# Performance work log

Measured on AMD Instinct MI355X. Metric: run time of the kernel, lower is better.

The kernel has to match this reference:

```python
import jax, jax.numpy as jnp
import numpy as np

EPS = 1e-7
BLOCK_SIZE = 128
LN_EPS = 1e-6

def _project(x):
    norm = jnp.maximum(jnp.linalg.norm(x, axis=-1, keepdims=True), EPS)
    max_norm = 1.0 - EPS
    return jnp.where(norm >= 1.0, x / norm * max_norm, x)

def _mobius_add(x, y, c):
    x2 = jnp.sum(x * x, -1, keepdims=True)
    y2 = jnp.sum(y * y, -1, keepdims=True)
    xy = jnp.sum(x * y, -1, keepdims=True)
    num = (1 + 2 * c * xy + c * y2) * x + (1 - c * x2) * y
    den = 1 + 2 * c * xy + c * c * x2 * y2
    return _project(num / jnp.maximum(den, EPS))

def _logmap0(y, c):
    sqrt_c = jnp.maximum(jnp.sqrt(c), EPS)
    y_norm = jnp.linalg.norm(y, axis=-1, keepdims=True)
    safe = jnp.maximum(y_norm, EPS)
    mag = jnp.arctanh(jnp.minimum(y_norm, 1.0 - EPS)) / sqrt_c
    return jnp.where(y_norm < EPS, jnp.zeros_like(y), mag * (y / safe))

def _expmap0(v, c):
    sqrt_c = jnp.maximum(jnp.sqrt(c), EPS)
    v_norm = jnp.linalg.norm(v, axis=-1, keepdims=True)
    safe = jnp.maximum(v_norm, EPS)
    mag = jnp.tanh(sqrt_c * safe) / sqrt_c
    return _project(jnp.where(v_norm < EPS, jnp.zeros_like(v), mag * (v / safe)))

def _dist(x, y, c):
    sqrt_c = jnp.maximum(jnp.sqrt(c), EPS)
    add_norm = jnp.linalg.norm(_mobius_add(-x, y, c), axis=-1)
    sc = jnp.squeeze(sqrt_c, -1)
    arg = jnp.minimum(sc * add_norm, 1.0 - EPS)
    return 2.0 * jnp.arctanh(arg) / sc

def _layernorm(t, scale, bias):
    mu = jnp.mean(t, -1, keepdims=True)
    var = jnp.mean((t - mu) ** 2, -1, keepdims=True)
    return (t - mu) * jax.lax.rsqrt(var + LN_EPS) * scale + bias

def _rope(x, fc):
    # x: [Be, H, bs, hd]; fc: [bs, hd//2] complex
    x_r, x_i = jnp.split(x, 2, -1)
    xc = jax.lax.complex(x_r, x_i)
    rot = xc * fc.reshape(1, 1, fc.shape[0], fc.shape[1])
    return jnp.concatenate([rot.real, rot.imag], -1)

def setup_inputs() -> dict:
    key = jax.random.key(0)
    ks = jax.random.split(key, 8)
    B, N, D, H = 1, 1024, 1024, 16
    w = lambda k, s: jax.random.normal(k, s, jnp.float32) * 0.02
    x = jax.random.normal(ks[0], (B, N, D), jnp.float32) * 0.02  # points inside the ball
    c_global = jax.random.uniform(ks[1], (B, 1), jnp.float32, minval=0.1, maxval=1.0)
    return dict(
        x=x, c_global=c_global,
        qkv_w=w(ks[2], (D, 3 * D)), qkv_b=jnp.zeros((3 * D,), jnp.float32),
        out_w=w(ks[3], (D, D)), out_b=jnp.zeros((D,), jnp.float32),
        ffn_w1=w(ks[4], (D, 4 * D)), ffn_b1=jnp.zeros((4 * D,), jnp.float32),
        ffn_w2=w(ks[5], (4 * D, D)), ffn_b2=jnp.zeros((D,), jnp.float32),
        ln1_scale=jnp.ones((D,), jnp.float32), ln1_bias=jnp.zeros((D,), jnp.float32),
        ln2_scale=jnp.ones((D,), jnp.float32), ln2_bias=jnp.zeros((D,), jnp.float32),
        c_logits=jnp.zeros((H,), jnp.float32),
        geo_scale=jnp.ones((1, H, 1, 1), jnp.float32),
        start_pos=0,
    )

def reference(x, c_global, qkv_w, qkv_b, out_w, out_b, ffn_w1, ffn_b1, ffn_w2, ffn_b2,
              ln1_scale, ln1_bias, ln2_scale, ln2_bias, c_logits, geo_scale, start_pos):
    B, N, D = x.shape
    H = c_logits.shape[0]
    hd = D // H
    bs = BLOCK_SIZE
    nb = N // bs
    Be = B * nb
    xb = x.reshape(Be, bs, D)
    c_b = jnp.repeat(c_global, nb, axis=0).reshape(Be, 1, 1)
    x_res1 = xb
    # tangent-space norm 1 + attention input
    x_norm = _expmap0(_layernorm(_logmap0(xb, c_b), ln1_scale, ln1_bias), c_b)
    x_tan = _logmap0(x_norm, c_b)
    qkv = (x_tan @ qkv_w + qkv_b).reshape(Be, bs, 3, H, hd).transpose(2, 0, 3, 1, 4)
    q, k, v = qkv[0], qkv[1], qkv[2]  # [Be, H, bs, hd]
    # block-local RoPE (module recomputes freqs_cis for h_dim/block_size internally)
    freqs = 1.0 / (10000.0 ** (jnp.arange(0, hd, 2, dtype=jnp.float32) / hd))
    fc = jnp.exp(1j * jnp.outer(jnp.arange(bs), freqs))
    q = _rope(q, fc)
    k = _rope(k, fc)
    c_head = jax.nn.softplus(c_logits).reshape(1, H, 1, 1)
    q_hyp = _expmap0(q, c_head)
    k_hyp = _expmap0(k, c_head)
    d = _dist(q_hyp[:, :, :, None, :], k_hyp[:, :, None, :, :], c_head[:, :, None, :, :])  # [Be,H,bs,bs]
    attn = jax.nn.softmax(-geo_scale * d, axis=-1)
    ao = jnp.einsum('bhqk,bhkd->bhqd', attn, v).transpose(0, 2, 1, 3).reshape(Be, bs, D)
    ao = ao @ out_w + out_b
    x_att = _mobius_add(x_res1, _expmap0(ao, c_b), c_b)
    # tangent-space norm 2 + hyperbolic FFN
    x_norm2 = _expmap0(_layernorm(_logmap0(x_att, c_b), ln2_scale, ln2_bias), c_b)
    t = _logmap0(x_norm2, c_b)
    t = jax.nn.gelu(t @ ffn_w1 + ffn_b1) @ ffn_w2 + ffn_b2
    x_ffn = _expmap0(t, c_b)
    out = _mobius_add(x_att, x_ffn, c_b)
    return out.reshape(B, N, D)
```

## Files before the change

kernel.cpp:

```cpp
#include <hip/hip_runtime.h>

typedef unsigned int uint;
typedef unsigned short ushort;
typedef __attribute__((ext_vector_type(8))) short bf16x8;
typedef __attribute__((ext_vector_type(4))) float f32x4;

#define EPSF 1e-7f
#define ONE_M_EPS 0.99999988079071044921875f
#define ATANH_1ME 8.4056213f
#define Y2_CLIP 0.99999982f

__device__ __forceinline__ ushort f2bf(float f){
  union{float f;uint u;}x; x.f=f; uint u=x.u;
  return (ushort)((u + 0x7fffu + ((u>>16)&1u)) >> 16);
}
__device__ __forceinline__ float bf2f(ushort u){
  union{uint u;float f;}x; x.u = ((uint)u)<<16; return x.f;
}
__device__ __forceinline__ float atanh_c(float a){
  a = fminf(a, ONE_M_EPS);
  return 0.5f*__logf((1.f+a)/(1.f-a));
}
__device__ __forceinline__ float gelu_t(float v){
  return 0.5f*v*(1.f + tanhf(0.7978845608f*(v + 0.044715f*v*v*v)));
}

__device__ __forceinline__ float expmap_factor(float n2, float sc, float& r2){
  float n = sqrtf(n2);
  if (n < EPSF) { r2 = 0.f; return 0.f; }
  float mag = tanhf(sc*n)/sc;
  float f = mag/n;
  if (mag >= 1.f) { f *= ONE_M_EPS/mag; r2 = Y2_CLIP; }
  else r2 = mag*mag;
  return f;
}
__device__ __forceinline__ float roundtrip_factor(float tn2, float sc){
  float tn = sqrtf(tn2);
  if (tn < EPSF) return 0.f;
  float mag = tanhf(sc*tn)/sc;
  if (mag >= 1.f) {
    return ATANH_1ME / (sc * tn);
  } else {
    if (mag < EPSF) return 0.f;
    return (mag/tn) * (atanh_c(mag) / (sc * mag));
  }
}

__device__ __constant__ float FREQS[32] = {
  1.0f, 0.7498942093324559f, 0.5623413251903491f, 0.4216965034285822f,
  0.31622776601683794f, 0.23713737056616552f, 0.1778279410038923f, 0.13335214321633242f,
  0.1f, 0.07498942093324558f, 0.05623413251903491f, 0.04216965034285822f,
  0.03162277660168379f, 0.023713737056616554f, 0.01778279410038923f, 0.013335214321633242f,
  0.01f, 0.007498942093324559f, 0.005623413251903491f, 0.004216965034285822f,
  0.0031622776601683794f, 0.0023713737056616554f, 0.0017782794100389228f, 0.0013335214321633241f,
  0.001f, 0.0007498942093324558f, 0.0005623413251903491f, 0.0004216965034285822f,
  0.00031622776601683794f, 0.00023713737056616553f, 0.00017782794100389227f, 0.00013335214321633243f
};

__device__ __forceinline__ float blkSum(float v, float* tmp){
  #pragma unroll
  for (int o=32;o>0;o>>=1) v += __shfl_xor(v, o, 64);
  int w = threadIdx.x >> 6;
  if ((threadIdx.x & 63) == 0) tmp[w] = v;
  __syncthreads();
  v = tmp[0]+tmp[1]+tmp[2]+tmp[3];
  __syncthreads();
  return v;
}
__device__ __forceinline__ float2 blkSum2(float a, float b, float* tmp){
  #pragma unroll
  for (int o=32;o>0;o>>=1){ a += __shfl_xor(a, o, 64); b += __shfl_xor(b, o, 64); }
  int w = threadIdx.x >> 6;
  if ((threadIdx.x & 63) == 0){ tmp[w] = a; tmp[4+w] = b; }
  __syncthreads();
  float2 r; r.x = tmp[0]+tmp[1]+tmp[2]+tmp[3]; r.y = tmp[4]+tmp[5]+tmp[6]+tmp[7];
  __syncthreads();
  return r;
}

__global__ __launch_bounds__(256) void k_pre(const float* __restrict__ qkv_w,
    const float* __restrict__ out_w, const float* __restrict__ ffn_w1,
    const float* __restrict__ ffn_w2, const float* __restrict__ x,
    const float* __restrict__ cg, const float* __restrict__ lns, const float* __restrict__ lnb,
    ushort* __restrict__ wq, ushort* __restrict__ wo,
    ushort* __restrict__ w1, ushort* __restrict__ w2, ushort* __restrict__ xtan){
  __shared__ float s[32][33];
  int b = blockIdx.x;
  if (b < 12288){
    const float* W; ushort* WT; int K, N;
    if (b < 3072){ W=qkv_w; WT=wq; K=1024; N=3072; }
    else if (b < 4096){ b-=3072; W=out_w; WT=wo; K=1024; N=1024; }
    else if (b < 8192){ b-=4096; W=ffn_w1; WT=w1; K=1024; N=4096; }
    else { b-=8192; W=ffn_w2; WT=w2; K=4096; N=1024; }
    int nbn = N >> 5;
    int n0 = (b % nbn)*32, k0 = (b / nbn)*32;
    int tx = threadIdx.x & 31, ty = threadIdx.x >> 5;
    #pragma unroll
    for (int i=0;i<4;i++)
      s[ty+8*i][tx] = W[(size_t)(k0+ty+8*i)*N + n0+tx];
    __syncthreads();
    #pragma unroll
    for (int i=0;i<4;i++)
      WT[(size_t)(n0+ty+8*i)*K + k0+tx] = f2bf(s[tx][ty+8*i]);
  } else {
    float* tmp = &s[0][0];
    int r = b - 12288, t = threadIdx.x;
    float c = cg[0];
    float sc = fmaxf(sqrtf(c), EPSF);
    float4 xv = ((const float4*)(x + (size_t)r*1024))[t];
    float n2 = blkSum(xv.x*xv.x + xv.y*xv.y + xv.z*xv.z + xv.w*xv.w, tmp);
    float n = sqrtf(n2);
    float f1 = (n < EPSF) ? 0.f : (atanh_c(n) / sc / n);
    float ux = xv.x*f1, uy = xv.y*f1, uz = xv.z*f1, uw = xv.w*f1;
    float2 s12 = blkSum2(ux+uy+uz+uw, ux*ux+uy*uy+uz*uz+uw*uw, tmp);
    float mu = s12.x*(1.f/1024.f);
    float var = s12.y*(1.f/1024.f) - mu*mu;
    float inv = rsqrtf(var + 1e-6f);
    float4 sv = ((const float4*)lns)[t];
    float4 bv = ((const float4*)lnb)[t];
    float ta = (ux-mu)*inv*sv.x + bv.x;
    float tb = (uy-mu)*inv*sv.y + bv.y;
    float tc = (uz-mu)*inv*sv.z + bv.z;
    float td = (uw-mu)*inv*sv.w + bv.w;
    float tn2 = blkSum(ta*ta+tb*tb+tc*tc+td*td, tmp);
    float f = roundtrip_factor(tn2, sc);
    ushort4 o; o.x=f2bf(ta*f); o.y=f2bf(tb*f); o.z=f2bf(tc*f); o.w=f2bf(td*f);
    ((ushort4*)(xtan + (size_t)r*1024))[t] = o;
  }
}

template<int EPI>
__global__ __launch_bounds__(256) void k_gemm(const ushort* __restrict__ A,
    const ushort* __restrict__ Bt, const float* __restrict__ bias,
    void* __restrict__ C, int M, int N, int Kstride, int Kchunk){
  constexpr int MF = 2, NF = 4;
  __shared__ ushort As[2][128*64];
  __shared__ ushort Bs[2][64*64];
  const int tid = threadIdx.x;
  const int lane = tid & 63;
  const int wid = tid >> 6;
  const int ro = wid * 32;
  const int l15 = lane & 15, hi = lane >> 4;
  const int nwg = gridDim.x * gridDim.y;
  const int lin = blockIdx.y * gridDim.x + blockIdx.x;
  const int qq = nwg >> 3, rr = nwg & 7;
  const int xcd = lin & 7, ii = lin >> 3;
  const int swz = (xcd < rr) ? (xcd*(qq+1) + ii) : (rr*(qq+1) + (xcd-rr)*qq + ii);
  const int m0 = (swz % gridDim.y) * 128;
  const int n0 = (swz / gridDim.y) * 64;
  const int z = blockIdx.z;
  const int kbase = z * Kchunk;
  const int swr = (l15 & 7) << 3;

  f32x4 acc[MF][NF];
  #pragma unroll
  for (int i=0;i<MF;i++)
    #pragma unroll
    for (int j=0;j<NF;j++) acc[i][j] = (f32x4){0.f,0.f,0.f,0.f};

  auto stage = [&](int buf, int koff){
    #pragma unroll
    for (int r2=0;r2<4;r2++){
      int idx = r2*256 + tid;
      int row = idx >> 3, cc = idx & 7;
      int off = koff + ((cc ^ (row & 7)) << 3);
      const ushort* ga = A + (size_t)(m0+row)*Kstride + off;
      int lo = (r2*256 + (tid & 192)) * 8;
      __builtin_amdgcn_global_load_lds((const __attribute__((address_space(1))) uint*)ga,
          (__attribute__((address_space(3))) uint*)&As[buf][lo], 16, 0, 0);
    }
    #pragma unroll
    for (int r2=0;r2<2;r2++){
      int idx = r2*256 + tid;
      int row = idx >> 3, cc = idx & 7;
      int off = koff + ((cc ^ (row & 7)) << 3);
      const ushort* gb = Bt + (size_t)(n0+row)*Kstride + off;
      int lo = (r2*256 + (tid & 192)) * 8;
      __builtin_amdgcn_global_load_lds((const __attribute__((address_space(1))) uint*)gb,
          (__attribute__((address_space(3))) uint*)&Bs[buf][lo], 16, 0, 0);
    }
  };
  auto compute = [&](int buf){
    #pragma unroll
    for (int ks=0;ks<2;ks++){
      bf16x8 af[MF], bfv[NF];
      int cb = (ks*32 + hi*8) ^ swr;
      #pragma unroll
      for (int m2=0;m2<MF;m2++) af[m2]  = *(const bf16x8*)&As[buf][(ro+m2*16+l15)*64 + cb];
      #pragma unroll
      for (int n2=0;n2<NF;n2++) bfv[n2] = *(const bf16x8*)&Bs[buf][(n2*16+l15)*64 + cb];
      #pragma unroll
      for (int m2=0;m2<MF;m2++)
        #pragma unroll
        for (int n2=0;n2<NF;n2++)
          acc[m2][n2] = __builtin_amdgcn_mfma_f32_16x16x32_bf16(af[m2], bfv[n2], acc[m2][n2], 0, 0, 0);
    }
  };

  const int nt = Kchunk >> 6;
  stage(0, kbase);
  __syncthreads();
  int cur = 0;
  for (int t = 1; t < nt; ++t){
    stage(cur ^ 1, kbase + t*64);
    compute(cur);
    __syncthreads();
    cur ^= 1;
  }
  compute(cur);

  #pragma unroll
  for (int m=0;m<MF;m++){
    #pragma unroll
    for (int n=0;n<NF;n++){
      int gc = n0 + n*16 + l15;
      float bb = (EPI == 3) ? (z == 0 ? bias[gc] : 0.f) : bias[gc];
      #pragma unroll
      for (int i=0;i<4;i++){
        int gr = m0 + ro + m*16 + hi*4 + i;
        float v = acc[m][n][i] + bb;
        if (EPI == 2) v = gelu_t(v);
        if (EPI == 2) ((ushort*)C)[(size_t)gr*N + gc] = f2bf(v);
        else ((float*)C)[(size_t)z*M*N + (size_t)gr*N + gc] = v;
      }
    }
  }
}

__global__ __launch_bounds__(256) void k_qkvprep(const float* __restrict__ qkv,
    const float* __restrict__ clog,
    ushort* __restrict__ qhg, ushort* __restrict__ qlg,
    ushort* __restrict__ khg, ushort* __restrict__ klg,
    ushort* __restrict__ vhg, float* __restrict__ q2g, float* __restrict__ k2g){
  constexpr size_t PSTRIDE = (size_t)1024*3072;
  const int gr = blockIdx.x;
  const int be = gr >> 7, r = gr & 127;
  const int t = threadIdx.x;
  const int h = t >> 4, d = t & 15;
  const float cl = clog[h];
  const float ch = (cl > 20.f) ? cl : log1pf(__expf(cl));
  const float sc = fmaxf(sqrtf(ch), EPSF);
  const float* base  = qkv + (size_t)gr*3072 + h*64;
  const float* base2 = base + PSTRIDE;
  const size_t rowbase = ((size_t)(be*16 + h)*128 + r)*64;
  const float fr = (float)r;
  #pragma unroll
  for (int qk=0; qk<2; qk++){
    int off = qk*1024;
    float v0 = base[off+d]    + base2[off+d];
    float v1 = base[off+d+16] + base2[off+d+16];
    float v2 = base[off+d+32] + base2[off+d+32];
    float v3 = base[off+d+48] + base2[off+d+48];
    float sn, cn;
    __sincosf(fr * FREQS[d], &sn, &cn);
    float a = v0, b = v2;
    v0 = a*cn - b*sn; v2 = a*sn + b*cn;
    __sincosf(fr * FREQS[d+16], &sn, &cn);
    a = v1; b = v3;
    v1 = a*cn - b*sn; v3 = a*sn + b*cn;
    float n2 = v0*v0 + v1*v1 + v2*v2 + v3*v3;
    #pragma unroll
    for (int o=1;o<16;o<<=1) n2 += __shfl_xor(n2, o);
    float r2; float f = expmap_factor(n2, sc, r2);
    ushort* hd = qk ? khg : qhg;
    ushort* ld = qk ? klg : qlg;
    float val;
    val = v0*f; ushort h0 = f2bf(val), l0 = f2bf(val - bf2f(h0));
    val = v1*f; ushort h1 = f2bf(val), l1 = f2bf(val - bf2f(h1));
    val = v2*f; ushort h2 = f2bf(val), l2 = f2bf(val - bf2f(h2));
    val = v3*f; ushort h3 = f2bf(val), l3 = f2bf(val - bf2f(h3));
    hd[rowbase+d]=h0; hd[rowbase+d+16]=h1; hd[rowbase+d+32]=h2; hd[rowbase+d+48]=h3;
    ld[rowbase+d]=l0; ld[rowbase+d+16]=l1; ld[rowbase+d+32]=l2; ld[rowbase+d+48]=l3;
    if (d == 0) (qk ? k2g : q2g)[(size_t)(be*16+h)*128 + r] = r2;
  }
  {
    float v0 = base[2048+d]    + base2[2048+d];
    float v1 = base[2048+d+16] + base2[2048+d+16];
    float v2 = base[2048+d+32] + base2[2048+d+32];
    float v3 = base[2048+d+48] + base2[2048+d+48];
    vhg[rowbase+d]    = f2bf(v0);
    vhg[rowbase+d+16] = f2bf(v1);
    vhg[rowbase+d+32] = f2bf(v2);
    vhg[rowbase+d+48] = f2bf(v3);
  }
}

__global__ __launch_bounds__(256) void k_attn6(const ushort* __restrict__ qhg,
    const ushort* __restrict__ qlg, const ushort* __restrict__ khg,
    const ushort* __restrict__ klg, const ushort* __restrict__ vhg,
    const float* __restrict__ q2g, const float* __restrict__ k2g,
    const float* __restrict__ c_logits, const float* __restrict__ geo,
    ushort* __restrict__ ao){
  __shared__ ushort Kh[128*64], Kl[128*64];
  __shared__ ushort Vth[64*128];
  __shared__ ushort Qh[64*64], Ql[64*64];
  __shared__ float k2s[128], q2s[64];
  const int h = blockIdx.x, be = blockIdx.y, qs = blockIdx.z;
  const int tid = threadIdx.x;
  const float cl = c_logits[h];
  const float ch = (cl > 20.f) ? cl : log1pf(__expf(cl));
  const float sc = fmaxf(sqrtf(ch), EPSF);
  const float gs = geo[h];
  const size_t tbase = (size_t)(be*16 + h)*8192;

  #pragma unroll
  for (int r2=0;r2<4;r2++){
    int idx = r2*256 + tid;
    int row = idx >> 3, cc = idx & 7;
    int off = row*64 + ((cc ^ (row & 7)) << 3);
    int lo = (r2*256 + (tid & 192)) * 8;
    __builtin_amdgcn_global_load_lds((const __attribute__((address_space(1))) uint*)(khg + tbase + off),
        (__attribute__((address_space(3))) uint*)&Kh[lo], 16, 0, 0);
    __builtin_amdgcn_global_load_lds((const __attribute__((address_space(1))) uint*)(klg + tbase + off),
        (__attribute__((address_space(3))) uint*)&Kl[lo], 16, 0, 0);
  }
  #pragma unroll
  for (int r2=0;r2<2;r2++){
    int idx = r2*256 + tid;
    int row = idx >> 3, cc = idx & 7;
    int off = (qs*64 + row)*64 + ((cc ^ (row & 7)) << 3);
    int lo = (r2*256 + (tid & 192)) * 8;
    __builtin_amdgcn_global_load_lds((const __attribute__((address_space(1))) uint*)(qhg + tbase + off),
        (__attribute__((address_space(3))) uint*)&Qh[lo], 16, 0, 0);
    __builtin_amdgcn_global_load_lds((const __attribute__((address_space(1))) uint*)(qlg + tbase + off),
        (__attribute__((address_space(3))) uint*)&Ql[lo], 16, 0, 0);
  }
  if (tid < 128){
    int kv = tid;
    const uint4* src = (const uint4*)(vhg + tbase + kv*64);
    ushort v[64];
    #pragma unroll
    for (int c2=0;c2<8;c2++) *(uint4*)&v[c2*8] = src[c2];
    #pragma unroll
    for (int d=0; d<64; d++){
      int idx = d*128 + (((kv>>3) ^ (d&7))<<3) + (kv&7);
      Vth[idx] = v[d];
    }
    k2s[kv] = k2g[(size_t)(be*16+h)*128 + kv];
  } else if (tid < 192){
    int i2 = tid - 128;
    q2s[i2] = q2g[(size_t)(be*16+h)*128 + qs*64 + i2];
  }
  __syncthreads();

  const int lane = tid & 63, w = tid >> 6;
  const int l15 = lane & 15, hi4 = lane >> 4;
  f32x4 acc[8];
  #pragma unroll
  for (int nf=0;nf<8;nf++) acc[nf] = (f32x4){0.f,0.f,0.f,0.f};
  #pragma unroll
  for (int ks=0; ks<2; ks++){
    int qrowL = w*16 + l15;
    int qidx = qrowL*64 + (((ks*4 + hi4) ^ (qrowL&7))<<3);
    bf16x8 qh = *(const bf16x8*)&Qh[qidx];
    bf16x8 ql2 = *(const bf16x8*)&Ql[qidx];
    #pragma unroll
    for (int nf=0; nf<8; nf++){
      int krow = nf*16 + l15;
      int kidx = krow*64 + (((ks*4 + hi4) ^ (krow&7))<<3);
      bf16x8 kh = *(const bf16x8*)&Kh[kidx];
      bf16x8 kl2 = *(const bf16x8*)&Kl[kidx];
      acc[nf] = __builtin_amdgcn_mfma_f32_16x16x32_bf16(qh, kh, acc[nf], 0, 0, 0);
      acc[nf] = __builtin_amdgcn_mfma_f32_16x16x32_bf16(qh, kl2, acc[nf], 0, 0, 0);
      acc[nf] = __builtin_amdgcn_mfma_f32_16x16x32_bf16(ql2, kh, acc[nf], 0, 0, 0);
    }
  }
  __syncthreads();

  float q2v[4], Bfv[4];
  #pragma unroll
  for (int i=0;i<4;i++){ q2v[i] = q2s[w*16 + hi4*4 + i]; Bfv[i] = 1.f - ch*q2v[i]; }
  const float e2 = 2.f*ch;
  #pragma unroll
  for (int nf=0; nf<8; nf++){
    float k2 = k2s[nf*16 + l15];
    #pragma unroll
    for (int i=0;i<4;i++){
      float xy = acc[nf][i];
      float Af = 1.f + ch*k2 - e2*xy;
      float den = fmaxf(Af - ch*k2*Bfv[i], EPSF);
      float num2 = fmaxf(Af*(Af*q2v[i] - 2.f*Bfv[i]*xy) + Bfv[i]*Bfv[i]*k2, 0.f);
      float rn = sqrtf(num2)/den;
      rn = (rn >= 1.f) ? ONE_M_EPS : rn;
      float arg = fminf(sc*rn, ONE_M_EPS);
      float dd = __logf((1.f+arg)/(1.f-arg)) / sc;
      acc[nf][i] = -gs*dd;
    }
  }
  #pragma unroll
  for (int i=0;i<4;i++){
    float m = acc[0][i];
    #pragma unroll
    for (int nf=1;nf<8;nf++) m = fmaxf(m, acc[nf][i]);
    #pragma unroll
    for (int o=1;o<16;o<<=1) m = fmaxf(m, __shfl_xor(m, o));
    float l = 0.f;
    #pragma unroll
    for (int nf=0;nf<8;nf++){ float pp = __expf(acc[nf][i]-m); acc[nf][i] = pp; l += pp; }
    #pragma unroll
    for (int o=1;o<16;o<<=1) l += __shfl_xor(l, o);
    float inv = 1.f/l;
    #pragma unroll
    for (int nf=0;nf<8;nf++){
      float p = acc[nf][i]*inv;
      ushort ph = f2bf(p);
      ushort pl = f2bf(p - bf2f(ph));
      int row = w*16 + hi4*4 + i, col = nf*16 + l15;
      int idx = row*128 + (((col>>3) ^ (row&7))<<3) + (col&7);
      Kh[idx] = ph; Kl[idx] = pl;
    }
  }
  __syncthreads();

  f32x4 acc2[4];
  #pragma unroll
  for (int nf=0;nf<4;nf++) acc2[nf] = (f32x4){0.f,0.f,0.f,0.f};
  #pragma unroll
  for (int ks=0; ks<4; ks++){
    int prow = w*16 + l15;
    int pidx = prow*128 + (((ks*4 + hi4) ^ (prow&7))<<3);
    bf16x8 ph = *(const bf16x8*)&Kh[pidx];
    bf16x8 pl = *(const bf16x8*)&Kl[pidx];
    #pragma unroll
    for (int nf=0; nf<4; nf++){
      int vrow = nf*16 + l15;
      int vidx = vrow*128 + (((ks*4 + hi4) ^ (vrow&7))<<3);
      bf16x8 vh = *(const bf16x8*)&Vth[vidx];
      acc2[nf] = __builtin_amdgcn_mfma_f32_16x16x32_bf16(ph, vh, acc2[nf], 0, 0, 0);
      acc2[nf] = __builtin_amdgcn_mfma_f32_16x16x32_bf16(pl, vh, acc2[nf], 0, 0, 0);
    }
  }
  #pragma unroll
  for (int nf=0; nf<4; nf++)
    #pragma unroll
    for (int i=0;i<4;i++){
      int row = qs*64 + w*16 + hi4*4 + i;
      int col = nf*16 + l15;
      ao[(size_t)(be*128 + row)*1024 + h*64 + col] = f2bf(acc2[nf][i]);
    }
}

__global__ __launch_bounds__(256) void k_postattn(const float* __restrict__ x,
    const float* __restrict__ proj, const float* __restrict__ cg,
    const float* __restrict__ lns, const float* __restrict__ lnb,
    float* __restrict__ xatt, ushort* __restrict__ tout){
  __shared__ float tmp[8];
  int r = blockIdx.x, t = threadIdx.x;
  float c = cg[0], sc = fmaxf(sqrtf(c), EPSF);
  float4 pa = ((const float4*)(proj + (size_t)r*1024))[t];
  float4 pb = ((const float4*)(proj + 1024*1024 + (size_t)r*1024))[t];
  float4 pc = ((const float4*)(proj + 2*1024*1024 + (size_t)r*1024))[t];
  float4 pd = ((const float4*)(proj + 3*1024*1024 + (size_t)r*1024))[t];
  float4 pv; pv.x=(pa.x+pb.x)+(pc.x+pd.x); pv.y=(pa.y+pb.y)+(pc.y+pd.y);
  pv.z=(pa.z+pb.z)+(pc.z+pd.z); pv.w=(pa.w+pb.w)+(pc.w+pd.w);
  float4 xv = ((const float4*)(x + (size_t)r*1024))[t];
  float pn2 = blkSum(pv.x*pv.x+pv.y*pv.y+pv.z*pv.z+pv.w*pv.w, tmp);
  float y2; float fy = expmap_factor(pn2, sc, y2);
  float ya = pv.x*fy, yb = pv.y*fy, yc = pv.z*fy, yd = pv.w*fy;
  float2 s = blkSum2(xv.x*xv.x+xv.y*xv.y+xv.z*xv.z+xv.w*xv.w,
                     xv.x*ya+xv.y*yb+xv.z*yc+xv.w*yd, tmp);
  float x2 = s.x, xy = s.y;
  float Af = 1.f + 2.f*c*xy + c*y2;
  float Bf = 1.f - c*x2;
  float den = fmaxf(1.f + 2.f*c*xy + c*c*x2*y2, EPSF);
  float num2 = fmaxf(Af*Af*x2 + 2.f*Af*Bf*xy + Bf*Bf*y2, 0.f);
  float rn = sqrtf(num2)/den;
  float fp = (rn >= 1.f) ? (ONE_M_EPS/fmaxf(rn,EPSF)) : 1.f;
  float xan = (rn >= 1.f) ? ONE_M_EPS : rn;
  float g = fp/den;
  float xa = (Af*xv.x + Bf*ya)*g;
  float xb = (Af*xv.y + Bf*yb)*g;
  float xc = (Af*xv.z + Bf*yc)*g;
  float xd = (Af*xv.w + Bf*yd)*g;
  float4 xo; xo.x=xa; xo.y=xb; xo.z=xc; xo.w=xd;
  ((float4*)(xatt + (size_t)r*1024))[t] = xo;
  float at = (rn >= 1.f) ? ATANH_1ME : atanh_c(xan);
  float fl = (xan < EPSF) ? 0.f : at / sc / fmaxf(xan, EPSF);
  float ux = xa*fl, uy = xb*fl, uz = xc*fl, uw = xd*fl;
  float2 s12 = blkSum2(ux+uy+uz+uw, ux*ux+uy*uy+uz*uz+uw*uw, tmp);
  float mu = s12.x*(1.f/1024.f);
  float var = s12.y*(1.f/1024.f) - mu*mu;
  float inv = rsqrtf(var + 1e-6f);
  float4 sv = ((const float4*)lns)[t];
  float4 bv = ((const float4*)lnb)[t];
  float ta = (ux-mu)*inv*sv.x + bv.x;
  float tb = (uy-mu)*inv*sv.y + bv.y;
  float tc = (uz-mu)*inv*sv.z + bv.z;
  float td = (uw-mu)*inv*sv.w + bv.w;
  float tn2 = blkSum(ta*ta+tb*tb+tc*tc+td*td, tmp);
  float f = roundtrip_factor(tn2, sc);
  ushort4 o; o.x=f2bf(ta*f); o.y=f2bf(tb*f); o.z=f2bf(tc*f); o.w=f2bf(td*f);
  ((ushort4*)(tout + (size_t)r*1024))[t] = o;
}

__global__ __launch_bounds__(256) void k_final(const float* __restrict__ xatt,
    const float* __restrict__ tf, const float* __restrict__ cg, float* __restrict__ out){
  __shared__ float tmp[8];
  int r = blockIdx.x, t = threadIdx.x;
  float c = cg[0], sc = fmaxf(sqrtf(c), EPSF);
  float4 fa = ((const float4*)(tf + (size_t)r*1024))[t];
  float4 fb = ((const float4*)(tf + 1024*1024 + (size_t)r*1024))[t];
  float4 fc = ((const float4*)(tf + 2*1024*1024 + (size_t)r*1024))[t];
  float4 fd = ((const float4*)(tf + 3*1024*1024 + (size_t)r*1024))[t];
  float4 fv; fv.x=(fa.x+fb.x)+(fc.x+fd.x); fv.y=(fa.y+fb.y)+(fc.y+fd.y);
  fv.z=(fa.z+fb.z)+(fc.z+fd.z); fv.w=(fa.w+fb.w)+(fc.w+fd.w);
  float4 xv = ((const float4*)(xatt + (size_t)r*1024))[t];
  float fn2 = blkSum(fv.x*fv.x+fv.y*fv.y+fv.z*fv.z+fv.w*fv.w, tmp);
  float y2; float fy = expmap_factor(fn2, sc, y2);
  float ya = fv.x*fy, yb = fv.y*fy, yc = fv.z*fy, yd = fv.w*fy;
  float2 s = blkSum2(xv.x*xv.x+xv.y*xv.y+xv.z*xv.z+xv.w*xv.w,
                     xv.x*ya+xv.y*yb+xv.z*yc+xv.w*yd, tmp);
  float x2 = s.x, xy = s.y;
  float Af = 1.f + 2.f*c*xy + c*y2;
  float Bf = 1.f - c*x2;
  float den = fmaxf(1.f + 2.f*c*xy + c*c*x2*y2, EPSF);
  float num2 = fmaxf(Af*Af*x2 + 2.f*Af*Bf*xy + Bf*Bf*y2, 0.f);
  float rn = sqrtf(num2)/den;
  float fp = (rn >= 1.f) ? (ONE_M_EPS/fmaxf(rn,EPSF)) : 1.f;
  float g = fp/den;
  float4 o;
  o.x = (Af*xv.x + Bf*ya)*g;
  o.y = (Af*xv.y + Bf*yb)*g;
  o.z = (Af*xv.z + Bf*yc)*g;
  o.w = (Af*xv.w + Bf*yd)*g;
  ((float4*)(out + (size_t)r*1024))[t] = o;
}

extern "C" void kernel_launch(void* const* d_in, const int* in_sizes, int n_in,
                              void* d_out, int out_size, void* d_ws, size_t ws_size,
                              hipStream_t stream){
  (void)in_sizes; (void)n_in; (void)out_size; (void)ws_size;
  const float* x     = (const float*)d_in[0];
  const float* cg    = (const float*)d_in[1];
  const float* qkv_w = (const float*)d_in[2];
  const float* qkv_b = (const float*)d_in[3];
  const float* out_w = (const float*)d_in[4];
  const float* out_b = (const float*)d_in[5];
  const float* ffn_w1= (const float*)d_in[6];
  const float* ffn_b1= (const float*)d_in[7];
  const float* ffn_w2= (const float*)d_in[8];
  const float* ffn_b2= (const float*)d_in[9];
  const float* ln1s  = (const float*)d_in[10];
  const float* ln1b  = (const float*)d_in[11];
  const float* ln2s  = (const float*)d_in[12];
  const float* ln2b  = (const float*)d_in[13];
  const float* clog  = (const float*)d_in[14];
  const float* geo   = (const float*)d_in[15];

  char* p = (char*)d_ws;
  auto take = [&](size_t n){ char* r = p; p += (n + 255) & ~(size_t)255; return r; };
  ushort* wt_qkv  = (ushort*)take((size_t)3072*1024*2);
  ushort* wt_out  = (ushort*)take((size_t)1024*1024*2);
  ushort* wt_ffn1 = (ushort*)take((size_t)4096*1024*2);
  ushort* wt_ffn2 = (ushort*)take((size_t)1024*4096*2);
  float*  bufA    = (float*)take((size_t)2*1024*3072*4);
  ushort* bufB    = (ushort*)take((size_t)1024*1024*2);
  float*  bufC    = (float*)take((size_t)4*1024*1024*4);
  float*  xatt    = (float*)take((size_t)1024*1024*4);
  ushort* tbuf    = (ushort*)take((size_t)1024*1024*2);
  ushort* qhg     = (ushort*)take((size_t)1024*1024*2);
  ushort* qlg     = (ushort*)take((size_t)1024*1024*2);
  ushort* khg     = (ushort*)take((size_t)1024*1024*2);
  ushort* klg     = (ushort*)take((size_t)1024*1024*2);
  ushort* vhg     = (ushort*)take((size_t)1024*1024*2);
  float*  q2g     = (float*)take((size_t)16384*4);
  float*  k2g     = (float*)take((size_t)16384*4);

  k_pre<<<13312, 256, 0, stream>>>(qkv_w, out_w, ffn_w1, ffn_w2, x, cg, ln1s, ln1b,
                                   wt_qkv, wt_out, wt_ffn1, wt_ffn2, bufB);
  k_gemm<3><<<dim3(48,8,2), 256, 0, stream>>>(bufB, wt_qkv, qkv_b, (void*)bufA, 1024, 3072, 1024, 512);
  k_qkvprep<<<1024, 256, 0, stream>>>(bufA, clog, qhg, qlg, khg, klg, vhg, q2g, k2g);
  k_attn6<<<dim3(16,8,2), 256, 0, stream>>>(qhg, qlg, khg, klg, vhg, q2g, k2g, clog, geo, bufB);
  k_gemm<3><<<dim3(16,8,4), 256, 0, stream>>>(bufB, wt_out, out_b, (void*)bufC, 1024, 1024, 1024, 256);
  k_postattn<<<1024, 256, 0, stream>>>(x, bufC, cg, ln2s, ln2b, xatt, tbuf);
  k_gemm<2><<<dim3(64,8,1), 256, 0, stream>>>(tbuf, wt_ffn1, ffn_b1, (void*)bufA, 1024, 4096, 1024, 1024);
  k_gemm<3><<<dim3(16,8,4), 256, 0, stream>>>((const ushort*)bufA, wt_ffn2, ffn_b2, (void*)bufC, 1024, 1024, 4096, 1024);
  k_final<<<1024, 256, 0, stream>>>(xatt, bufC, cg, (float*)d_out);
}
```

Measured before the change: 117.6 us.

## Overlap out/FFN weight transpose-conversion with QKV GEMM via extra grid blocks

Moves the fp32-to-bf16 transpose of the out, FFN1 and FFN2 weights out of the pre-kernel and into extra blocks appended to the QKV GEMM grid. Those blocks run the transpose and exit while the GEMM blocks compute, so the bandwidth-bound conversion can overlap the compute-bound GEMM. The pre-kernel shrinks to QKV weight conversion plus the row prep. The cost is that the extra blocks compete with GEMM tiles for CUs and bandwidth, and block scheduling order decides how much overlap actually happens.

```diff
diff --git a/kernel.cpp b/kernel.cpp
--- a/kernel.cpp
+++ b/kernel.cpp
@@ -78,33 +78,29 @@
   return r;
 }
 
+__device__ __forceinline__ void tcvt32(const float* __restrict__ W, ushort* __restrict__ WT,
+                                       int K, int N, int n0, int k0, float (*s)[33]){
+  int tx = threadIdx.x & 31, ty = threadIdx.x >> 5;
+  #pragma unroll
+  for (int i=0;i<4;i++)
+    s[ty+8*i][tx] = W[(size_t)(k0+ty+8*i)*N + n0+tx];
+  __syncthreads();
+  #pragma unroll
+  for (int i=0;i<4;i++)
+    WT[(size_t)(n0+ty+8*i)*K + k0+tx] = f2bf(s[tx][ty+8*i]);
+}
+
 __global__ __launch_bounds__(256) void k_pre(const float* __restrict__ qkv_w,
-    const float* __restrict__ out_w, const float* __restrict__ ffn_w1,
-    const float* __restrict__ ffn_w2, const float* __restrict__ x,
+    const float* __restrict__ x,
     const float* __restrict__ cg, const float* __restrict__ lns, const float* __restrict__ lnb,
-    ushort* __restrict__ wq, ushort* __restrict__ wo,
-    ushort* __restrict__ w1, ushort* __restrict__ w2, ushort* __restrict__ xtan){
+    ushort* __restrict__ wq, ushort* __restrict__ xtan){
   __shared__ float s[32][33];
   int b = blockIdx.x;
-  if (b < 12288){
-    const float* W; ushort* WT; int K, N;
-    if (b < 3072){ W=qkv_w; WT=wq; K=1024; N=3072; }
-    else if (b < 4096){ b-=3072; W=out_w; WT=wo; K=1024; N=1024; }
-    else if (b < 8192){ b-=4096; W=ffn_w1; WT=w1; K=1024; N=4096; }
-    else { b-=8192; W=ffn_w2; WT=w2; K=4096; N=1024; }
-    int nbn = N >> 5;
-    int n0 = (b % nbn)*32, k0 = (b / nbn)*32;
-    int tx = threadIdx.x & 31, ty = threadIdx.x >> 5;
-    #pragma unroll
-    for (int i=0;i<4;i++)
-      s[ty+8*i][tx] = W[(size_t)(k0+ty+8*i)*N + n0+tx];
-    __syncthreads();
-    #pragma unroll
-    for (int i=0;i<4;i++)
-      WT[(size_t)(n0+ty+8*i)*K + k0+tx] = f2bf(s[tx][ty+8*i]);
+  if (b < 3072){
+    tcvt32(qkv_w, wq, 1024, 3072, (b % 96)*32, (b / 96)*32, s);
   } else {
     float* tmp = &s[0][0];
-    int r = b - 12288, t = threadIdx.x;
+    int r = b - 3072, t = threadIdx.x;
     float c = cg[0];
     float sc = fmaxf(sqrtf(c), EPSF);
     float4 xv = ((const float4*)(x + (size_t)r*1024))[t];
@@ -129,20 +125,35 @@
   }
 }
 
-template<int EPI>
+template<int EPI, bool FUSE_T = false>
 __global__ __launch_bounds__(256) void k_gemm(const ushort* __restrict__ A,
     const ushort* __restrict__ Bt, const float* __restrict__ bias,
-    void* __restrict__ C, int M, int N, int Kstride, int Kchunk){
+    void* __restrict__ C, int M, int N, int Kstride, int Kchunk,
+    const float* __restrict__ out_w = nullptr, const float* __restrict__ ffn_w1 = nullptr,
+    const float* __restrict__ ffn_w2 = nullptr, ushort* __restrict__ wo = nullptr,
+    ushort* __restrict__ w1 = nullptr, ushort* __restrict__ w2 = nullptr){
   constexpr int MF = 2, NF = 4;
+  constexpr int GX = 48;
   __shared__ ushort As[2][128*64];
   __shared__ ushort Bs[2][64*64];
+
+  if (FUSE_T && blockIdx.x >= GX){
+    float (*s)[33] = (float(*)[33])&As[0][0];
+    int tb = (blockIdx.x - GX) + 576*(blockIdx.y*2 + blockIdx.z);
+    if (tb < 1024)      tcvt32(out_w,  wo, 1024, 1024, (tb % 32)*32,  (tb / 32)*32, s);
+    else if (tb < 5120){ tb -= 1024;  tcvt32(ffn_w1, w1, 1024, 4096, (tb % 128)*32, (tb / 128)*32, s); }
+    else               { tb -= 5120;  tcvt32(ffn_w2, w2, 4096, 1024, (tb % 32)*32,  (tb / 32)*32, s); }
+    return;
+  }
+
   const int tid = threadIdx.x;
   const int lane = tid & 63;
   const int wid = tid >> 6;
   const int ro = wid * 32;
   const int l15 = lane & 15, hi = lane >> 4;
-  const int nwg = gridDim.x * gridDim.y;
-  const int lin = blockIdx.y * gridDim.x + blockIdx.x;
+  const int gx = FUSE_T ? GX : gridDim.x;
+  const int nwg = gx * gridDim.y;
+  const int lin = blockIdx.y * gx + blockIdx.x;
   const int qq = nwg >> 3, rr = nwg & 7;
   const int xcd = lin & 7, ii = lin >> 3;
   const int swz = (xcd < rr) ? (xcd*(qq+1) + ii) : (rr*(qq+1) + (xcd-rr)*qq + ii);
@@ -566,9 +577,9 @@
   float*  q2g     = (float*)take((size_t)16384*4);
   float*  k2g     = (float*)take((size_t)16384*4);
 
-  k_pre<<<13312, 256, 0, stream>>>(qkv_w, out_w, ffn_w1, ffn_w2, x, cg, ln1s, ln1b,
-                                   wt_qkv, wt_out, wt_ffn1, wt_ffn2, bufB);
-  k_gemm<3><<<dim3(48,8,2), 256, 0, stream>>>(bufB, wt_qkv, qkv_b, (void*)bufA, 1024, 3072, 1024, 512);
+  k_pre<<<4096, 256, 0, stream>>>(qkv_w, x, cg, ln1s, ln1b, wt_qkv, bufB);
+  k_gemm<3, true><<<dim3(48+576, 8, 2), 256, 0, stream>>>(bufB, wt_qkv, qkv_b, (void*)bufA,
+      1024, 3072, 1024, 512, out_w, ffn_w1, ffn_w2, wt_out, wt_ffn1, wt_ffn2);
   k_qkvprep<<<1024, 256, 0, stream>>>(bufA, clog, qhg, qlg, khg, klg, vhg, q2g, k2g);
   k_attn6<<<dim3(16,8,2), 256, 0, stream>>>(qhg, qlg, khg, klg, vhg, q2g, k2g, clog, geo, bufB);
   k_gemm<3><<<dim3(16,8,4), 256, 0, stream>>>(bufB, wt_out, out_b, (void*)bufC, 1024, 1024, 1024, 256);
```

Result: slower. 123.9 us (+5.3%).

## Shrink GEMM tile to 64x64 and drop split-K for QKV projection

Applied to the files above, without the earlier changes.

The GEMM kernel's M tile drops from 128 to 64 rows, so each wave now computes one 16-row fragment. Grids double in the M dimension to give more workgroups on the GPU. The QKV projection no longer uses two-way split-K, so the prep kernel reads a single partial instead of summing two, and the workspace buffer shrinks. The trade-off is more parallelism and less partial-sum traffic against lower per-tile data reuse and more redundant B-tile loads.

```diff
diff --git a/kernel.cpp b/kernel.cpp
--- a/kernel.cpp
+++ b/kernel.cpp
@@ -133,67 +133,55 @@
 __global__ __launch_bounds__(256) void k_gemm(const ushort* __restrict__ A,
     const ushort* __restrict__ Bt, const float* __restrict__ bias,
     void* __restrict__ C, int M, int N, int Kstride, int Kchunk){
-  constexpr int MF = 2, NF = 4;
-  __shared__ ushort As[2][128*64];
+  constexpr int NF = 4;
+  __shared__ ushort As[2][64*64];
   __shared__ ushort Bs[2][64*64];
   const int tid = threadIdx.x;
   const int lane = tid & 63;
   const int wid = tid >> 6;
-  const int ro = wid * 32;
+  const int ro = wid * 16;
   const int l15 = lane & 15, hi = lane >> 4;
   const int nwg = gridDim.x * gridDim.y;
   const int lin = blockIdx.y * gridDim.x + blockIdx.x;
   const int qq = nwg >> 3, rr = nwg & 7;
   const int xcd = lin & 7, ii = lin >> 3;
   const int swz = (xcd < rr) ? (xcd*(qq+1) + ii) : (rr*(qq+1) + (xcd-rr)*qq + ii);
-  const int m0 = (swz % gridDim.y) * 128;
+  const int m0 = (swz % gridDim.y) * 64;
   const int n0 = (swz / gridDim.y) * 64;
   const int z = blockIdx.z;
   const int kbase = z * Kchunk;
   const int swr = (l15 & 7) << 3;
 
-  f32x4 acc[MF][NF];
-  #pragma unroll
-  for (int i=0;i<MF;i++)
-    #pragma unroll
-    for (int j=0;j<NF;j++) acc[i][j] = (f32x4){0.f,0.f,0.f,0.f};
+  f32x4 acc[NF];
+  #pragma unroll
+  for (int j=0;j<NF;j++) acc[j] = (f32x4){0.f,0.f,0.f,0.f};
 
   auto stage = [&](int buf, int koff){
-    #pragma unroll
-    for (int r2=0;r2<4;r2++){
-      int idx = r2*256 + tid;
-      int row = idx >> 3, cc = idx & 7;
-      int off = koff + ((cc ^ (row & 7)) << 3);
-      const ushort* ga = A + (size_t)(m0+row)*Kstride + off;
-      int lo = (r2*256 + (tid & 192)) * 8;
-      __builtin_amdgcn_global_load_lds((const __attribute__((address_space(1))) uint*)ga,
-          (__attribute__((address_space(3))) uint*)&As[buf][lo], 16, 0, 0);
-    }
     #pragma unroll
     for (int r2=0;r2<2;r2++){
       int idx = r2*256 + tid;
       int row = idx >> 3, cc = idx & 7;
       int off = koff + ((cc ^ (row & 7)) << 3);
-      const ushort* gb = Bt + (size_t)(n0+row)*Kstride + off;
       int lo = (r2*256 + (tid & 192)) * 8;
-      __builtin_amdgcn_global_load_lds((const __attribute__((address_space(1))) uint*)gb,
+      __builtin_amdgcn_global_load_lds((const __attribute__((address_space(1))) uint*)
+          (A + (size_t)(m0+row)*Kstride + off),
+          (__attribute__((address_space(3))) uint*)&As[buf][lo], 16, 0, 0);
+      __builtin_amdgcn_global_load_lds((const __attribute__((address_space(1))) uint*)
+          (Bt + (size_t)(n0+row)*Kstride + off),
           (__attribute__((address_space(3))) uint*)&Bs[buf][lo], 16, 0, 0);
     }
   };
   auto compute = [&](int buf){
     #pragma unroll
     for (int ks=0;ks<2;ks++){
-      bf16x8 af[MF], bfv[NF];
+      bf16x8 af, bfv[NF];
       int cb = (ks*32 + hi*8) ^ swr;
-      #pragma unroll
-      for (int m2=0;m2<MF;m2++) af[m2]  = *(const bf16x8*)&As[buf][(ro+m2*16+l15)*64 + cb];
+      af = *(const bf16x8*)&As[buf][(ro+l15)*64 + cb];
       #pragma unroll
       for (int n2=0;n2<NF;n2++) bfv[n2] = *(const bf16x8*)&Bs[buf][(n2*16+l15)*64 + cb];
       #pragma unroll
-      for (int m2=0;m2<MF;m2++)
-        #pragma unroll
-        for (int n2=0;n2<NF;n2++)
-          acc[m2][n2] = __builtin_amdgcn_mfma_f32_16x16x32_bf16(af[m2], bfv[n2], acc[m2][n2], 0, 0, 0);
+      for (int n2=0;n2<NF;n2++)
+        acc[n2] = __builtin_amdgcn_mfma_f32_16x16x32_bf16(af, bfv[n2], acc[n2], 0, 0, 0);
     }
   };
 
@@ -210,19 +198,16 @@
   compute(cur);
 
   #pragma unroll
-  for (int m=0;m<MF;m++){
-    #pragma unroll
-    for (int n=0;n<NF;n++){
-      int gc = n0 + n*16 + l15;
-      float bb = (EPI == 3) ? (z == 0 ? bias[gc] : 0.f) : bias[gc];
-      #pragma unroll
-      for (int i=0;i<4;i++){
-        int gr = m0 + ro + m*16 + hi*4 + i;
-        float v = acc[m][n][i] + bb;
-        if (EPI == 2) v = gelu_t(v);
-        if (EPI == 2) ((ushort*)C)[(size_t)gr*N + gc] = f2bf(v);
-        else ((float*)C)[(size_t)z*M*N + (size_t)gr*N + gc] = v;
-      }
+  for (int n=0;n<NF;n++){
+    int gc = n0 + n*16 + l15;
+    float bb = (EPI == 3) ? (z == 0 ? bias[gc] : 0.f) : bias[gc];
+    #pragma unroll
+    for (int i=0;i<4;i++){
+      int gr = m0 + ro + hi*4 + i;
+      float v = acc[n][i] + bb;
+      if (EPI == 2) v = gelu_t(v);
+      if (EPI == 2) ((ushort*)C)[(size_t)gr*N + gc] = f2bf(v);
+      else ((float*)C)[(size_t)z*M*N + (size_t)gr*N + gc] = v;
     }
   }
 }
@@ -232,7 +217,6 @@
     ushort* __restrict__ qhg, ushort* __restrict__ qlg,
     ushort* __restrict__ khg, ushort* __restrict__ klg,
     ushort* __restrict__ vhg, float* __restrict__ q2g, float* __restrict__ k2g){
-  constexpr size_t PSTRIDE = (size_t)1024*3072;
   const int gr = blockIdx.x;
   const int be = gr >> 7, r = gr & 127;
   const int t = threadIdx.x;
@@ -240,17 +224,16 @@
   const float cl = clog[h];
   const float ch = (cl > 20.f) ? cl : log1pf(__expf(cl));
   const float sc = fmaxf(sqrtf(ch), EPSF);
-  const float* base  = qkv + (size_t)gr*3072 + h*64;
-  const float* base2 = base + PSTRIDE;
+  const float* base = qkv + (size_t)gr*3072 + h*64;
   const size_t rowbase = ((size_t)(be*16 + h)*128 + r)*64;
   const float fr = (float)r;
   #pragma unroll
   for (int qk=0; qk<2; qk++){
     int off = qk*1024;
-    float v0 = base[off+d]    + base2[off+d];
-    float v1 = base[off+d+16] + base2[off+d+16];
-    float v2 = base[off+d+32] + base2[off+d+32];
-    float v3 = base[off+d+48] + base2[off+d+48];
+    float v0 = base[off+d];
+    float v1 = base[off+d+16];
+    float v2 = base[off+d+32];
+    float v3 = base[off+d+48];
     float sn, cn;
     __sincosf(fr * FREQS[d], &sn, &cn);
     float a = v0, b = v2;
@@ -274,14 +257,10 @@
     if (d == 0) (qk ? k2g : q2g)[(size_t)(be*16+h)*128 + r] = r2;
   }
   {
-    float v0 = base[2048+d]    + base2[2048+d];
-    float v1 = base[2048+d+16] + base2[2048+d+16];
-    float v2 = base[2048+d+32] + base2[2048+d+32];
-    float v3 = base[2048+d+48] + base2[2048+d+48];
-    vhg[rowbase+d]    = f2bf(v0);
-    vhg[rowbase+d+16] = f2bf(v1);
-    vhg[rowbase+d+32] = f2bf(v2);
-    vhg[rowbase+d+48] = f2bf(v3);
+    vhg[rowbase+d]    = f2bf(base[2048+d]);
+    vhg[rowbase+d+16] = f2bf(base[2048+d+16]);
+    vhg[rowbase+d+32] = f2bf(base[2048+d+32]);
+    vhg[rowbase+d+48] = f2bf(base[2048+d+48]);
   }
 }
 
@@ -553,7 +532,7 @@
   ushort* wt_out  = (ushort*)take((size_t)1024*1024*2);
   ushort* wt_ffn1 = (ushort*)take((size_t)4096*1024*2);
   ushort* wt_ffn2 = (ushort*)take((size_t)1024*4096*2);
-  float*  bufA    = (float*)take((size_t)2*1024*3072*4);
+  float*  bufA    = (float*)take((size_t)1024*3072*4);
   ushort* bufB    = (ushort*)take((size_t)1024*1024*2);
   float*  bufC    = (float*)take((size_t)4*1024*1024*4);
   float*  xatt    = (float*)take((size_t)1024*1024*4);
@@ -568,12 +547,12 @@
 
   k_pre<<<13312, 256, 0, stream>>>(qkv_w, out_w, ffn_w1, ffn_w2, x, cg, ln1s, ln1b,
                                    wt_qkv, wt_out, wt_ffn1, wt_ffn2, bufB);
-  k_gemm<3><<<dim3(48,8,2), 256, 0, stream>>>(bufB, wt_qkv, qkv_b, (void*)bufA, 1024, 3072, 1024, 512);
+  k_gemm<3><<<dim3(48,16,1), 256, 0, stream>>>(bufB, wt_qkv, qkv_b, (void*)bufA, 1024, 3072, 1024, 1024);
   k_qkvprep<<<1024, 256, 0, stream>>>(bufA, clog, qhg, qlg, khg, klg, vhg, q2g, k2g);
   k_attn6<<<dim3(16,8,2), 256, 0, stream>>>(qhg, qlg, khg, klg, vhg, q2g, k2g, clog, geo, bufB);
-  k_gemm<3><<<dim3(16,8,4), 256, 0, stream>>>(bufB, wt_out, out_b, (void*)bufC, 1024, 1024, 1024, 256);
+  k_gemm<3><<<dim3(16,16,4), 256, 0, stream>>>(bufB, wt_out, out_b, (void*)bufC, 1024, 1024, 1024, 256);
   k_postattn<<<1024, 256, 0, stream>>>(x, bufC, cg, ln2s, ln2b, xatt, tbuf);
-  k_gemm<2><<<dim3(64,8,1), 256, 0, stream>>>(tbuf, wt_ffn1, ffn_b1, (void*)bufA, 1024, 4096, 1024, 1024);
-  k_gemm<3><<<dim3(16,8,4), 256, 0, stream>>>((const ushort*)bufA, wt_ffn2, ffn_b2, (void*)bufC, 1024, 1024, 4096, 1024);
+  k_gemm<2><<<dim3(64,16,1), 256, 0, stream>>>(tbuf, wt_ffn1, ffn_b1, (void*)bufA, 1024, 4096, 1024, 1024);
+  k_gemm<3><<<dim3(16,16,4), 256, 0, stream>>>((const ushort*)bufA, wt_ffn2, ffn_b2, (void*)bufC, 1024, 1024, 4096, 1024);
   k_final<<<1024, 256, 0, stream>>>(xatt, bufC, cg, (float*)d_out);
 }
```

Result: faster. 113.3 us (-3.7%).
